# Kernel tuning notes

Hardware: AMD Instinct MI355X
Metric: run time of the kernel (lower is better)

The kernel has to match this reference:

```python
import jax, jax.numpy as jnp
import numpy as np

NBASIS = 128
CUTOFF = 6.0
N_NODES = 50000
N_EDGES = 800000
DEG = 4

# RBFExpansion(vmax=cutoff, bins=nbasis): centers on [0, cutoff], gamma = 1/mean spacing
CENTERS = jnp.linspace(0.0, CUTOFF, NBASIS)
GAMMA = 1.0 / (CUTOFF / (NBASIS - 1))
# PolynomialEmbeddingFunction(degree=4, use_sqrt_term=True)
POWERS = jnp.concatenate([jnp.array([0.5], dtype=jnp.float32), 1.0 + jnp.arange(DEG, dtype=jnp.float32)])
SF = jnp.concatenate([jnp.array([2.0], dtype=jnp.float32),
                      1.0 / 10.0 ** jnp.cumsum(jnp.log10(1.0 + jnp.arange(DEG, dtype=jnp.float32)))])


def _spline(bond, phi, use_softplus):
    # bond: [E]; phi: [NBASIS, 1] -> [E, 1]
    fc = 0.5 * (1.0 + jnp.cos(np.pi * bond / CUTOFF))  # cosine cutoff fcut(r)
    b = jnp.exp(-GAMMA * (bond[:, None] - CENTERS) ** 2) * (0.5 * fc)[:, None]  # [E, NBASIS]
    coeff = jax.nn.softplus(phi) if use_softplus else phi
    return b @ coeff  # (b.unsqueeze(-1) * act(phi)).sum(dim=1)


def _energy(r, phi_density, phi_pair, emb_weights, src, dst):
    bond = jnp.linalg.norm(r, axis=1)  # [E]
    dens_ij = _spline(bond, phi_density, True)  # [E, 1], softplus-activated spline
    local = jax.ops.segment_sum(dens_ij, dst, num_segments=N_NODES)  # copy_e + sum -> [N, 1]
    basis = local[..., None] ** POWERS  # [N, 1, P]
    F = jnp.einsum('ndp,pd->nd', basis, emb_weights * SF[:, None])  # embedding energy [N, 1]
    pair = _spline(bond, phi_pair, False) / bond[:, None]  # pair repulsion / r, [E, 1]
    return F.sum() + pair.sum()  # readout_nodes + readout_edges (single graph)


def setup_inputs() -> dict:
    key = jax.random.key(0)
    k1, k2, k3, k4, k5, k6 = jax.random.split(key, 6)
    # scale so bond lengths stay well inside the 6.0 cutoff
    r = 0.8 * jax.random.normal(k1, (N_EDGES, 3), dtype=jnp.float32)
    src = jax.random.randint(k2, (N_EDGES,), 0, N_NODES)
    dst = jax.random.randint(k3, (N_EDGES,), 0, N_NODES)
    phi_density = 0.1 * jax.random.normal(k4, (NBASIS, 1), dtype=jnp.float32)
    phi_pair = 0.1 * jax.random.normal(k5, (NBASIS, 1), dtype=jnp.float32)
    emb_weights = 0.1 * jax.random.normal(k6, (DEG + 1, 1), dtype=jnp.float32)
    return {"r": r, "src": src, "dst": dst, "phi_density": phi_density,
            "phi_pair": phi_pair, "emb_weights": emb_weights}


def reference(r, src, dst, phi_density, phi_pair, emb_weights):
    energy, dE_dr = jax.value_and_grad(_energy, argnums=0)(
        r, phi_density, phi_pair, emb_weights, src, dst)
    # autograd_forces: r_ij = x_dst - x_src, force_i = -dE/dx_i
    forces = (jax.ops.segment_sum(dE_dr, src, num_segments=N_NODES)
              - jax.ops.segment_sum(dE_dr, dst, num_segments=N_NODES))
    return energy, forces
```

## Files before the change

### kernel.cpp

```cpp
#include <hip/hip_runtime.h>
#include <cmath>

#define NB 128
static constexpr float CUT  = 6.0f;
static constexpr float STEP = CUT / (NB - 1);
static constexpr float GAM  = (NB - 1) / CUT;
static constexpr float PIF  = 3.14159265358979f;

__device__ __forceinline__ float4 spline_eval(float u,
                                              const float* __restrict__ spd,
                                              const float* __restrict__ pp) {
    float ang  = u * (PIF / CUT);
    float s    = __sinf(ang);
    float c    = __cosf(ang);
    float fc2  = 0.25f * (1.0f + c);
    float dfc2 = -0.25f * (PIF / CUT) * s;
    float dens = 0.f, ddens = 0.f, pair = 0.f, dpair = 0.f;
#pragma unroll 8
    for (int k = 0; k < NB; ++k) {
        float d   = u - k * STEP;
        float ek  = __expf(-GAM * d * d);
        float dek = -2.0f * GAM * d * ek;
        float bk  = ek * fc2;
        float dbk = fmaf(dek, fc2, ek * dfc2);
        dens  = fmaf(bk,  spd[k], dens);
        ddens = fmaf(dbk, spd[k], ddens);
        pair  = fmaf(bk,  pp[k],  pair);
        dpair = fmaf(dbk, pp[k],  dpair);
    }
    return make_float4(dens, ddens, pair, dpair);
}

__device__ __forceinline__ void block_reduce_add(float v, float* target) {
#pragma unroll
    for (int o = 32; o > 0; o >>= 1) v += __shfl_down(v, o, 64);
    __shared__ float wsum[8];
    int lane = threadIdx.x & 63;
    int wid  = threadIdx.x >> 6;
    if (lane == 0) wsum[wid] = v;
    __syncthreads();
    if (threadIdx.x == 0) {
        float s = 0.f;
        int nw = (blockDim.x + 63) >> 6;
        for (int i = 0; i < nw; ++i) s += wsum[i];
        atomicAdd(target, s);
    }
}

template <bool STORE>
__global__ void edge_pass1(const float* __restrict__ r,
                           const int*   __restrict__ dst,
                           const float* __restrict__ phi_d,
                           const float* __restrict__ phi_p,
                           float* __restrict__ local,
                           float* __restrict__ A,
                           float* __restrict__ B,
                           float* __restrict__ energy,
                           int E) {
    __shared__ float spd[NB], pp[NB];
    int t = threadIdx.x;
    if (t < NB) {
        spd[t] = log1pf(__expf(phi_d[t]));
        pp[t]  = phi_p[t];
    }
    __syncthreads();
    int e = blockIdx.x * blockDim.x + t;
    float epair = 0.f;
    if (e < E) {
        float x = r[3*e+0], y = r[3*e+1], z = r[3*e+2];
        float u = sqrtf(fmaf(x, x, fmaf(y, y, z*z)));
        float4 q = spline_eval(u, spd, pp);
        float inv = 1.0f / u;
        atomicAdd(&local[dst[e]], q.x);
        if (STORE) {
            A[e] = q.y * inv;
            B[e] = (q.w - q.z * inv) * inv * inv;
        }
        epair = q.z * inv;
    }
    block_reduce_add(epair, energy);
}

__global__ void node_pass(const float* __restrict__ local,
                          const float* __restrict__ w,
                          float* __restrict__ Fp,
                          float* __restrict__ energy,
                          int N) {
    int n = blockIdx.x * blockDim.x + threadIdx.x;
    float Fv = 0.f;
    if (n < N) {
        float x  = local[n];
        float w0 = w[0], w1 = w[1], w2 = w[2], w3 = w[3], w4 = w[4];
        float sq = sqrtf(x);
        float x2 = x * x;
        Fv = 2.f*w0*sq + w1*x + 0.5f*w2*x2 + (1.f/6.f)*w3*x2*x + (1.f/24.f)*w4*x2*x2;
        Fp[n] = w0 / sq + w1 + w2*x + 0.5f*w3*x2 + (1.f/6.f)*w4*x2*x;
    }
    block_reduce_add(Fv, energy);
}

template <bool STORE>
__global__ void edge_pass2(const float* __restrict__ r,
                           const int*   __restrict__ src,
                           const int*   __restrict__ dst,
                           const float* __restrict__ A,
                           const float* __restrict__ B,
                           const float* __restrict__ Fp,
                           const float* __restrict__ phi_d,
                           const float* __restrict__ phi_p,
                           float* __restrict__ forces,
                           int E) {
    __shared__ float spd[NB], pp[NB];
    if (!STORE) {
        int t = threadIdx.x;
        if (t < NB) {
            spd[t] = log1pf(__expf(phi_d[t]));
            pp[t]  = phi_p[t];
        }
        __syncthreads();
    }
    int e = blockIdx.x * blockDim.x + threadIdx.x;
    if (e >= E) return;
    float x = r[3*e+0], y = r[3*e+1], z = r[3*e+2];
    int sn = src[e], dn = dst[e];
    float g;
    if (STORE) {
        g = fmaf(Fp[dn], A[e], B[e]);
    } else {
        float u = sqrtf(fmaf(x, x, fmaf(y, y, z*z)));
        float4 q = spline_eval(u, spd, pp);
        float inv = 1.0f / u;
        g = Fp[dn] * (q.y * inv) + (q.w - q.z * inv) * inv * inv;
    }
    float fx = g * x, fy = g * y, fz = g * z;
    atomicAdd(&forces[3*sn+0],  fx);
    atomicAdd(&forces[3*sn+1],  fy);
    atomicAdd(&forces[3*sn+2],  fz);
    atomicAdd(&forces[3*dn+0], -fx);
    atomicAdd(&forces[3*dn+1], -fy);
    atomicAdd(&forces[3*dn+2], -fz);
}

extern "C" void kernel_launch(void* const* d_in, const int* in_sizes, int n_in,
                              void* d_out, int out_size, void* d_ws, size_t ws_size,
                              hipStream_t stream) {
    const float* r     = (const float*)d_in[0];
    const int*   src   = (const int*)  d_in[1];
    const int*   dst   = (const int*)  d_in[2];
    const float* phi_d = (const float*)d_in[3];
    const float* phi_p = (const float*)d_in[4];
    const float* w     = (const float*)d_in[5];
    float* out = (float*)d_out;

    int E = in_sizes[1];
    int N = (out_size - 1) / 3;

    float* local = (float*)d_ws;
    float* Fp    = local + N;
    float* A     = Fp + N;
    float* B     = A + E;
    size_t need  = (size_t)(2 * N + 2 * E) * sizeof(float);
    bool store = ws_size >= need;

    hipMemsetAsync(d_out, 0, (size_t)out_size * sizeof(float), stream);
    hipMemsetAsync(local, 0, (size_t)N * sizeof(float), stream);

    int be = (E + 255) / 256;
    int bn = (N + 255) / 256;

    if (store) {
        edge_pass1<true ><<<be, 256, 0, stream>>>(r, dst, phi_d, phi_p, local, A, B, out, E);
    } else {
        edge_pass1<false><<<be, 256, 0, stream>>>(r, dst, phi_d, phi_p, local, nullptr, nullptr, out, E);
    }
    node_pass<<<bn, 256, 0, stream>>>(local, w, Fp, out, N);
    if (store) {
        edge_pass2<true ><<<be, 256, 0, stream>>>(r, src, dst, A, B, Fp, phi_d, phi_p, out + 1, E);
    } else {
        edge_pass2<false><<<be, 256, 0, stream>>>(r, src, dst, nullptr, nullptr, Fp, phi_d, phi_p, out + 1, E);
    }
}
```

Measured before the change: 328.6 us.

## Truncate RBF sum to local window, interleave coeffs, use unsafe atomics

The spline evaluation now sums only a 48-center window around each bond length instead of all 128 Gaussians. The cut is justified by the large gamma, which makes distant terms negligible. Coefficients are packed as float2 in shared memory and the distance update is incremental. Float atomics switch to unsafeAtomicAdd to get hardware FP atomics on MI-series GPUs, and the non-store fallback path is removed. As a result the code now assumes the workspace is large enough and introduces a small truncation error.

Result: faster. 321.2 us (-2.2%).

```diff
diff --git a/kernel.cpp b/kernel.cpp
--- a/kernel.cpp
+++ b/kernel.cpp
@@ -2,33 +2,53 @@
 #include <cmath>
 
 #define NB 128
+#define WIN 48
 static constexpr float CUT  = 6.0f;
 static constexpr float STEP = CUT / (NB - 1);
 static constexpr float GAM  = (NB - 1) / CUT;
 static constexpr float PIF  = 3.14159265358979f;
 
-__device__ __forceinline__ float4 spline_eval(float u,
-                                              const float* __restrict__ spd,
-                                              const float* __restrict__ pp) {
+__device__ __forceinline__ void atomic_add_f32(float* p, float v) {
+    unsafeAtomicAdd(p, v);
+}
+
+__device__ __forceinline__ float4 spline_eval(float u, const float2* __restrict__ co) {
     float ang  = u * (PIF / CUT);
     float s    = __sinf(ang);
     float c    = __cosf(ang);
     float fc2  = 0.25f * (1.0f + c);
     float dfc2 = -0.25f * (PIF / CUT) * s;
+    int k0 = (int)ceilf((u - 1.1f) * (1.0f / STEP));
+    k0 = max(0, min(NB - WIN, k0));
+    float d = u - k0 * STEP;
     float dens = 0.f, ddens = 0.f, pair = 0.f, dpair = 0.f;
 #pragma unroll 8
-    for (int k = 0; k < NB; ++k) {
-        float d   = u - k * STEP;
+    for (int j = 0; j < WIN; ++j) {
+        float2 w  = co[k0 + j];
         float ek  = __expf(-GAM * d * d);
         float dek = -2.0f * GAM * d * ek;
         float bk  = ek * fc2;
         float dbk = fmaf(dek, fc2, ek * dfc2);
-        dens  = fmaf(bk,  spd[k], dens);
-        ddens = fmaf(dbk, spd[k], ddens);
-        pair  = fmaf(bk,  pp[k],  pair);
-        dpair = fmaf(dbk, pp[k],  dpair);
+        dens  = fmaf(bk,  w.x, dens);
+        ddens = fmaf(dbk, w.x, ddens);
+        pair  = fmaf(bk,  w.y, pair);
+        dpair = fmaf(dbk, w.y, dpair);
+        d -= STEP;
     }
     return make_float4(dens, ddens, pair, dpair);
+}
+
+__device__ __forceinline__ void load_coeffs(const float* __restrict__ phi_d,
+                                            const float* __restrict__ phi_p,
+                                            float2* co) {
+    int t = threadIdx.x;
+    if (t < NB) {
+        float2 w;
+        w.x = log1pf(__expf(phi_d[t]));
+        w.y = phi_p[t];
+        co[t] = w;
+    }
+    __syncthreads();
 }
 
 __device__ __forceinline__ void block_reduce_add(float v, float* target) {
@@ -43,11 +63,10 @@
         float s = 0.f;
         int nw = (blockDim.x + 63) >> 6;
         for (int i = 0; i < nw; ++i) s += wsum[i];
-        atomicAdd(target, s);
+        atomic_add_f32(target, s);
     }
 }
 
-template <bool STORE>
 __global__ void edge_pass1(const float* __restrict__ r,
                            const int*   __restrict__ dst,
                            const float* __restrict__ phi_d,
@@ -57,25 +76,18 @@
                            float* __restrict__ B,
                            float* __restrict__ energy,
                            int E) {
-    __shared__ float spd[NB], pp[NB];
-    int t = threadIdx.x;
-    if (t < NB) {
-        spd[t] = log1pf(__expf(phi_d[t]));
-        pp[t]  = phi_p[t];
-    }
-    __syncthreads();
-    int e = blockIdx.x * blockDim.x + t;
+    __shared__ float2 co[NB];
+    load_coeffs(phi_d, phi_p, co);
+    int e = blockIdx.x * blockDim.x + threadIdx.x;
     float epair = 0.f;
     if (e < E) {
         float x = r[3*e+0], y = r[3*e+1], z = r[3*e+2];
         float u = sqrtf(fmaf(x, x, fmaf(y, y, z*z)));
-        float4 q = spline_eval(u, spd, pp);
+        float4 q = spline_eval(u, co);
         float inv = 1.0f / u;
-        atomicAdd(&local[dst[e]], q.x);
-        if (STORE) {
-            A[e] = q.y * inv;
-            B[e] = (q.w - q.z * inv) * inv * inv;
-        }
+        atomic_add_f32(&local[dst[e]], q.x);
+        A[e] = q.y * inv;
+        B[e] = (q.w - q.z * inv) * inv * inv;
         epair = q.z * inv;
     }
     block_reduce_add(epair, energy);
@@ -99,46 +111,26 @@
     block_reduce_add(Fv, energy);
 }
 
-template <bool STORE>
 __global__ void edge_pass2(const float* __restrict__ r,
                            const int*   __restrict__ src,
                            const int*   __restrict__ dst,
                            const float* __restrict__ A,
                            const float* __restrict__ B,
                            const float* __restrict__ Fp,
-                           const float* __restrict__ phi_d,
-                           const float* __restrict__ phi_p,
                            float* __restrict__ forces,
                            int E) {
-    __shared__ float spd[NB], pp[NB];
-    if (!STORE) {
-        int t = threadIdx.x;
-        if (t < NB) {
-            spd[t] = log1pf(__expf(phi_d[t]));
-            pp[t]  = phi_p[t];
-        }
-        __syncthreads();
-    }
     int e = blockIdx.x * blockDim.x + threadIdx.x;
     if (e >= E) return;
     float x = r[3*e+0], y = r[3*e+1], z = r[3*e+2];
     int sn = src[e], dn = dst[e];
-    float g;
-    if (STORE) {
-        g = fmaf(Fp[dn], A[e], B[e]);
-    } else {
-        float u = sqrtf(fmaf(x, x, fmaf(y, y, z*z)));
-        float4 q = spline_eval(u, spd, pp);
-        float inv = 1.0f / u;
-        g = Fp[dn] * (q.y * inv) + (q.w - q.z * inv) * inv * inv;
-    }
+    float g = fmaf(Fp[dn], A[e], B[e]);
     float fx = g * x, fy = g * y, fz = g * z;
-    atomicAdd(&forces[3*sn+0],  fx);
-    atomicAdd(&forces[3*sn+1],  fy);
-    atomicAdd(&forces[3*sn+2],  fz);
-    atomicAdd(&forces[3*dn+0], -fx);
-    atomicAdd(&forces[3*dn+1], -fy);
-    atomicAdd(&forces[3*dn+2], -fz);
+    atomic_add_f32(&forces[3*sn+0],  fx);
+    atomic_add_f32(&forces[3*sn+1],  fy);
+    atomic_add_f32(&forces[3*sn+2],  fz);
+    atomic_add_f32(&forces[3*dn+0], -fx);
+    atomic_add_f32(&forces[3*dn+1], -fy);
+    atomic_add_f32(&forces[3*dn+2], -fz);
 }
 
 extern "C" void kernel_launch(void* const* d_in, const int* in_sizes, int n_in,
@@ -159,8 +151,6 @@
     float* Fp    = local + N;
     float* A     = Fp + N;
     float* B     = A + E;
-    size_t need  = (size_t)(2 * N + 2 * E) * sizeof(float);
-    bool store = ws_size >= need;
 
     hipMemsetAsync(d_out, 0, (size_t)out_size * sizeof(float), stream);
     hipMemsetAsync(local, 0, (size_t)N * sizeof(float), stream);
@@ -168,15 +158,7 @@
     int be = (E + 255) / 256;
     int bn = (N + 255) / 256;
 
-    if (store) {
-        edge_pass1<true ><<<be, 256, 0, stream>>>(r, dst, phi_d, phi_p, local, A, B, out, E);
-    } else {
-        edge_pass1<false><<<be, 256, 0, stream>>>(r, dst, phi_d, phi_p, local, nullptr, nullptr, out, E);
-    }
-    node_pass<<<bn, 256, 0, stream>>>(local, w, Fp, out, N);
-    if (store) {
-        edge_pass2<true ><<<be, 256, 0, stream>>>(r, src, dst, A, B, Fp, phi_d, phi_p, out + 1, E);
-    } else {
-        edge_pass2<false><<<be, 256, 0, stream>>>(r, src, dst, nullptr, nullptr, Fp, phi_d, phi_p, out + 1, E);
-    }
+    edge_pass1<<<be, 256, 0, stream>>>(r, dst, phi_d, phi_p, local, A, B, out, E);
+    node_pass <<<bn, 256, 0, stream>>>(local, w, Fp, out, N);
+    edge_pass2<<<be, 256, 0, stream>>>(r, src, dst, A, B, Fp, out + 1, E);
 }
```
